# Kernel tuning notes

Measured on AMD Instinct MI355X. Metric: run time of the kernel, lower is better.

The kernel has to match this reference:

```python
import jax, jax.numpy as jnp
import numpy as np


def setup_inputs() -> dict:
    key = jax.random.key(0)
    ks = jax.random.split(key, 6)
    B, C, H, W = 4, 512, 64, 64
    Ci = C // 2
    x = jax.random.normal(ks[0], (B, C, H, W), dtype=jnp.float32)
    # 1x1 conv weights (kaiming-ish scale)
    wq = jax.random.normal(ks[1], (Ci, C), dtype=jnp.float32) * np.float32(np.sqrt(2.0 / C))
    wk = jax.random.normal(ks[2], (Ci, C), dtype=jnp.float32) * np.float32(np.sqrt(2.0 / C))
    wv = jax.random.normal(ks[3], (C, C), dtype=jnp.float32) * np.float32(np.sqrt(2.0 / C))
    bq = jnp.zeros((Ci,), jnp.float32)
    bk = jnp.zeros((Ci,), jnp.float32)
    bv = jnp.zeros((C,), jnp.float32)
    gamma_pam = jax.random.uniform(ks[4], (1,), dtype=jnp.float32)
    gamma_cam = jax.random.uniform(ks[5], (1,), dtype=jnp.float32)
    return {"x": x, "wq": wq, "bq": bq, "wk": wk, "bk": bk,
            "wv": wv, "bv": bv, "gamma_pam": gamma_pam, "gamma_cam": gamma_cam}


def reference(x, wq, bq, wk, bk, wv, bv, gamma_pam, gamma_cam):
    B, C, H, W = x.shape
    N = H * W
    xf = x.reshape(B, C, N)  # [B,C,N]

    # ---- PAM (position attention) ----
    q = jnp.einsum('oc,bcn->bon', wq, xf) + bq[None, :, None]  # [B,C/2,N]
    k = jnp.einsum('oc,bcn->bon', wk, xf) + bk[None, :, None]  # [B,C/2,N]
    v = jnp.einsum('oc,bcn->bon', wv, xf) + bv[None, :, None]  # [B,C,N]
    # energy[b,i,j] = sum_c q[b,c,i] k[b,c,j] / sqrt(C)
    energy = jnp.einsum('bci,bcj->bij', q, k) / jnp.sqrt(jnp.float32(C))
    attn = jax.nn.softmax(energy, axis=-1) / jnp.float32(N)  # [B,N,N]
    # out[b,c,i] = sum_j v[b,c,j] * attn[i,j]
    pam_out = jnp.einsum('bcj,bij->bci', v, attn)
    sa = jnp.tanh(gamma_pam[0] * pam_out + xf)  # [B,C,N]

    # ---- CAM (channel attention) on sa ----
    energy_c = jnp.einsum('bcn,bdn->bcd', sa, sa) / jnp.sqrt(jnp.float32(N))  # [B,C,C]
    energy_new = jnp.max(energy_c, axis=-1, keepdims=True) - energy_c
    attn_c = jax.nn.softmax(energy_new, axis=-1) / jnp.float32(C)
    cam_out = jnp.einsum('bcd,bdn->bcn', attn_c, sa)
    out = gamma_cam[0] * cam_out + sa
    return out.reshape(B, C, H, W)
```

## Files before the change

### kernel.cpp

```cpp
#include <hip/hip_runtime.h>

#define B_ 4
#define C_ 512
#define CI_ 256
#define N_ 4096
#define SCALE_PAM 0.04419417382415922f
#define SCALE_CAM (1.0f/64.0f)
#define SHIFT_PAM 8.0f

typedef float v4f __attribute__((ext_vector_type(4)));
typedef short v8s __attribute__((ext_vector_type(8)));

__device__ __forceinline__ unsigned short f2bf(float f) {
  unsigned int u = __float_as_uint(f);
  u = (u + 0x7FFFu + ((u >> 16) & 1u)) >> 16;
  return (unsigned short)u;
}
__device__ __forceinline__ float bf2f(unsigned short s) {
  return __uint_as_float(((unsigned int)s) << 16);
}
__device__ __forceinline__ v8s ld8(const unsigned short* p) {
  v8s r; *(int4*)&r = *(const int4*)p; return r;
}
__device__ __forceinline__ v4f mfma16(v8s a, v8s b, v4f c) {
  return __builtin_amdgcn_mfma_f32_16x16x32_bf16(a, b, c, 0, 0, 0);
}

__global__ __launch_bounds__(256) void k_wb(const float* __restrict__ wq,
                                            const float* __restrict__ wk,
                                            const float* __restrict__ wv,
                                            unsigned short* __restrict__ w_pk) {
  int u = blockIdx.x * 256 + threadIdx.x;
  int blk = u >> 6, wi = (u & 63) * 8;
  int r = (blk >> 4) * 16 + (wi >> 5);
  int k = (blk & 15) * 32 + (wi & 31);
  const float* src = (r < 256) ? &wq[r * 512 + k]
                   : (r < 512) ? &wk[(r - 256) * 512 + k]
                               : &wv[(r - 512) * 512 + k];
  float4 f0 = *(const float4*)src, f1 = *(const float4*)(src + 4);
  ushort4 o0 = { f2bf(f0.x), f2bf(f0.y), f2bf(f0.z), f2bf(f0.w) };
  ushort4 o1 = { f2bf(f1.x), f2bf(f1.y), f2bf(f1.z), f2bf(f1.w) };
  *(ushort4*)&w_pk[u * 8] = o0;
  *(ushort4*)&w_pk[u * 8 + 4] = o1;
}

__global__ __launch_bounds__(256) void k_xT(const float* __restrict__ x,
                                            unsigned short* __restrict__ x_pk) {
  const int b = blockIdx.z, c0 = blockIdx.y * 64, n0 = blockIdx.x * 64;
  const int t = threadIdx.x;
  __shared__ unsigned short ts[64 * 72];
  const int cl = t >> 2, nseg = (t & 3) * 16;
  const float* xr = x + ((size_t)b * C_ + c0 + cl) * N_ + n0 + nseg;
#pragma unroll
  for (int k = 0; k < 4; ++k) {
    float4 f = *(const float4*)(xr + k * 4);
    ts[(nseg + k * 4 + 0) * 72 + cl] = f2bf(f.x);
    ts[(nseg + k * 4 + 1) * 72 + cl] = f2bf(f.y);
    ts[(nseg + k * 4 + 2) * 72 + cl] = f2bf(f.z);
    ts[(nseg + k * 4 + 3) * 72 + cl] = f2bf(f.w);
  }
  __syncthreads();
  unsigned short* dst = x_pk + (size_t)b * N_ * C_;
#pragma unroll
  for (int u = t; u < 512; u += 256) {
    int blk = u >> 6, wi = (u & 63) * 8;
    int rl = (blk >> 1) * 16 + (wi >> 5);
    int kl = (blk & 1) * 32 + (wi & 31);
    int gr = n0 + rl, gk = c0 + kl;
    size_t go = ((size_t)(gr >> 4) * 16 + (gk >> 5)) * 512 + (gr & 15) * 32 + (gk & 31);
    *(int4*)&dst[go] = *(int4*)&ts[rl * 72 + kl];
  }
}

__global__ __launch_bounds__(512) void k_qkv(
    const unsigned short* __restrict__ w_pk, const unsigned short* __restrict__ x_pk,
    const float* __restrict__ bq, const float* __restrict__ bk, const float* __restrict__ bv,
    unsigned short* __restrict__ q_pk, unsigned short* __restrict__ k_pk,
    unsigned short* __restrict__ v_pk) {
  const int b = blockIdx.z, o0 = blockIdx.y * 128, n0 = blockIdx.x * 128;
  const int t = threadIdx.x, wave = t >> 6, lane = t & 63;
  const int la = lane & 15, quad = lane >> 4;
  const int ow = wave & 1, nw = wave >> 1;
  const int lanelin = la * 32 + quad * 8;
  const unsigned short* xpb = x_pk + (size_t)b * N_ * C_;
  __shared__ unsigned short tp[128 * 136];

  v4f acc[4][2];
#pragma unroll
  for (int i = 0; i < 4; ++i)
#pragma unroll
    for (int j = 0; j < 2; ++j) acc[i][j] = (v4f){0.f, 0.f, 0.f, 0.f};

  const int ar16 = (o0 + ow * 64) >> 4;
  const int br16 = (n0 + nw * 32) >> 4;
#pragma unroll 4
  for (int s = 0; s < 16; ++s) {
    v8s b0 = ld8(&xpb[((size_t)(br16 + 0) * 16 + s) * 512 + lanelin]);
    v8s b1 = ld8(&xpb[((size_t)(br16 + 1) * 16 + s) * 512 + lanelin]);
#pragma unroll
    for (int oi = 0; oi < 4; ++oi) {
      v8s a = ld8(&w_pk[((size_t)(ar16 + oi) * 16 + s) * 512 + lanelin]);
      acc[oi][0] = mfma16(a, b0, acc[oi][0]);
      acc[oi][1] = mfma16(a, b1, acc[oi][1]);
    }
  }

  if (o0 >= 512) {
#pragma unroll
    for (int oi = 0; oi < 4; ++oi)
#pragma unroll
      for (int nj = 0; nj < 2; ++nj)
#pragma unroll
        for (int r = 0; r < 4; ++r) {
          int cl = ow * 64 + oi * 16 + quad * 4 + r;
          int nl = nw * 32 + nj * 16 + la;
          tp[cl * 136 + nl] = f2bf(acc[oi][nj][r] + bv[o0 - 512 + cl]);
        }
    __syncthreads();
    unsigned short* dst = v_pk + (size_t)b * C_ * N_;
#pragma unroll
    for (int u = t; u < 2048; u += 512) {
      int blk = u >> 6, wi = (u & 63) * 8;
      int rl = (blk >> 2) * 16 + (wi >> 5);
      int kl = (blk & 3) * 32 + (wi & 31);
      int gr = (o0 - 512) + rl, gk = n0 + kl;
      size_t go = ((size_t)(gr >> 4) * 128 + (gk >> 5)) * 512 + (gr & 15) * 32 + (gk & 31);
      *(int4*)&dst[go] = *(int4*)&tp[rl * 136 + kl];
    }
  } else {
    const float* bias = (o0 < 256) ? bq : bk;
#pragma unroll
    for (int oi = 0; oi < 4; ++oi)
#pragma unroll
      for (int nj = 0; nj < 2; ++nj)
#pragma unroll
        for (int r = 0; r < 4; ++r) {
          int ol = ow * 64 + oi * 16 + quad * 4 + r;
          int nl = nw * 32 + nj * 16 + la;
          tp[nl * 136 + ol] = f2bf(acc[oi][nj][r] + bias[(o0 & 255) + ol]);
        }
    __syncthreads();
    unsigned short* dst = ((o0 < 256) ? q_pk : k_pk) + (size_t)b * N_ * CI_;
#pragma unroll
    for (int u = t; u < 2048; u += 512) {
      int blk = u >> 6, wi = (u & 63) * 8;
      int rl = (blk >> 2) * 16 + (wi >> 5);
      int kl = (blk & 3) * 32 + (wi & 31);
      int gr = n0 + rl, gk = (o0 & 255) + kl;
      size_t go = ((size_t)(gr >> 4) * 8 + (gk >> 5)) * 512 + (gr & 15) * 32 + (gk & 31);
      *(int4*)&dst[go] = *(int4*)&tp[rl * 136 + kl];
    }
  }
}

__device__ __forceinline__ void kstage(const unsigned short* g, unsigned short* l, int t) {
  __builtin_amdgcn_global_load_lds(
      (const __attribute__((address_space(1))) void*)(g + (size_t)t * 8),
      (__attribute__((address_space(3))) void*)(l + t * 8), 16, 0, 0);
  __builtin_amdgcn_global_load_lds(
      (const __attribute__((address_space(1))) void*)(g + 8192 + (size_t)t * 8),
      (__attribute__((address_space(3))) void*)(l + 8192 + t * 8), 16, 0, 0);
}

__global__ __launch_bounds__(1024) void k_pam(
    const unsigned short* __restrict__ q_pk, const unsigned short* __restrict__ k_pk,
    const unsigned short* __restrict__ v_pk, const float* __restrict__ x,
    const float* __restrict__ gamma_pam,
    unsigned short* __restrict__ sa_pk, unsigned short* __restrict__ saT_pk) {
  const int blk = blockIdx.x;
  const int b = blk & 3, i0 = (blk >> 2) * 64;
  const int t = threadIdx.x, wave = t >> 6, lane = t & 63;
  const int la = lane & 15, quad = lane >> 4;
  const int iw = wave & 3, jw = wave >> 2;
  const int cb = wave * 32;
  const int lanelin = la * 32 + quad * 8;

  __shared__ unsigned short kls[3][16384];
  __shared__ unsigned short pa[2][4096];
  __shared__ float l_lds[64];
  if (t < 64) l_lds[t] = 0.f;

  const unsigned short* qpk = q_pk + (size_t)b * N_ * CI_;
  const unsigned short* kpk = k_pk + (size_t)b * N_ * CI_;
  const unsigned short* vpk = v_pk + (size_t)b * C_ * N_;

  v8s qf[8];
  {
    const unsigned short* qb = qpk + ((size_t)((i0 >> 4) + iw) * 8) * 512 + lanelin;
#pragma unroll
    for (int s = 0; s < 8; ++s) qf[s] = ld8(qb + s * 512);
  }

  v4f acc[2][4];
#pragma unroll
  for (int ct = 0; ct < 2; ++ct)
#pragma unroll
    for (int it = 0; it < 4; ++it) acc[ct][it] = (v4f){0.f, 0.f, 0.f, 0.f};
  float lsum[4] = {0.f, 0.f, 0.f, 0.f};

  kstage(kpk, kls[0], t);
  kstage(kpk + (size_t)4 * 4096, kls[1], t);
  asm volatile("s_waitcnt vmcnt(2)" ::: "memory");
  __builtin_amdgcn_s_barrier();
  __builtin_amdgcn_sched_barrier(0);

  int pb = 0;
  for (int step = 0; step < 64; ++step) {
    const int j0 = step * 64;
    v8s vf[2][2];
#pragma unroll
    for (int ct = 0; ct < 2; ++ct)
#pragma unroll
      for (int ks = 0; ks < 2; ++ks)
        vf[ct][ks] = ld8(&vpk[((size_t)((cb >> 4) + ct) * 128 + (j0 >> 5) + ks) * 512 + lanelin]);
    __builtin_amdgcn_sched_barrier(0);
    int jn = j0 + 128; if (jn >= N_) jn = 0;
    kstage(kpk + (size_t)(jn >> 4) * 4096, kls[(step + 2) % 3], t);
    __builtin_amdgcn_sched_barrier(0);
    const unsigned short* kb = &kls[step % 3][jw * 4096 + lanelin];
    v4f sA = (v4f){0.f, 0.f, 0.f, 0.f}, sB = sA;
#pragma unroll
    for (int sh = 0; sh < 4; ++sh) {
      sA = mfma16(qf[sh], ld8(kb + sh * 512), sA);
      sB = mfma16(qf[sh + 4], ld8(kb + (sh + 4) * 512), sB);
    }
#pragma unroll
    for (int r = 0; r < 4; ++r) {
      float p = __expf((sA[r] + sB[r]) * SCALE_PAM - SHIFT_PAM);
      lsum[r] += p;
      int row = iw * 16 + quad * 4 + r;
      pa[pb][((row << 6) + jw * 16 + la) ^ ((row & 7) << 3)] = f2bf(p);
    }
    __builtin_amdgcn_sched_barrier(0);
    asm volatile("s_waitcnt lgkmcnt(0) vmcnt(6)" ::: "memory");
    __builtin_amdgcn_s_barrier();
    __builtin_amdgcn_sched_barrier(0);
    __builtin_amdgcn_s_setprio(1);
#pragma unroll
    for (int it = 0; it < 4; ++it) {
      const int row = it * 16 + la;
      const int sw = (row & 7) << 3;
#pragma unroll
      for (int ks = 0; ks < 2; ++ks) {
        v8s pf; *(int4*)&pf = *(const int4*)&pa[pb][((row << 6) + ks * 32 + quad * 8) ^ sw];
#pragma unroll
        for (int ct = 0; ct < 2; ++ct)
          acc[ct][it] = mfma16(vf[ct][ks], pf, acc[ct][it]);
      }
    }
    __builtin_amdgcn_s_setprio(0);
    pb ^= 1;
  }

#pragma unroll
  for (int r = 0; r < 4; ++r) {
    float v = lsum[r];
    v += __shfl_xor(v, 1); v += __shfl_xor(v, 2);
    v += __shfl_xor(v, 4); v += __shfl_xor(v, 8);
    if (la == 0) atomicAdd(&l_lds[iw * 16 + quad * 4 + r], v);
  }
  __syncthreads();

  const float gpv = gamma_pam[0];
  unsigned short* ts = &kls[0][0];
  unsigned short sv[2][4][4];
#pragma unroll
  for (int ct = 0; ct < 2; ++ct)
#pragma unroll
    for (int it = 0; it < 4; ++it) {
      const int nl = it * 16 + la;
      const float lv = l_lds[nl] * (float)N_;
#pragma unroll
      for (int r = 0; r < 4; ++r) {
        const int c = cb + ct * 16 + quad * 4 + r;
        const float xv = x[((size_t)b * C_ + c) * N_ + i0 + nl];
        const unsigned short h = f2bf(tanhf(fmaf(gpv, acc[ct][it][r] / lv, xv)));
        sv[ct][it][r] = h;
        ts[c * 72 + nl] = h;
      }
    }
  __syncthreads();
  {
    unsigned short* dst = sa_pk + (size_t)b * C_ * N_;
#pragma unroll
    for (int u = t; u < 4096; u += 1024) {
      int c = u >> 3, n8 = (u & 7) * 8;
      int gn = i0 + n8;
      size_t go = ((size_t)(c >> 4) * 128 + (gn >> 5)) * 512 + (c & 15) * 32 + (gn & 31);
      *(int4*)&dst[go] = *(const int4*)&ts[c * 72 + n8];
    }
  }
  __syncthreads();
  unsigned short* ts2 = &kls[0][0];
#pragma unroll
  for (int ct = 0; ct < 2; ++ct)
#pragma unroll
    for (int it = 0; it < 4; ++it)
#pragma unroll
      for (int r = 0; r < 4; ++r)
        ts2[(it * 16 + la) * 520 + (cb + ct * 16 + quad * 4 + r)] = sv[ct][it][r];
  __syncthreads();
  {
    unsigned short* dst = saT_pk + (size_t)b * N_ * C_;
#pragma unroll
    for (int u = t; u < 4096; u += 1024) {
      int nl = u >> 6, c8 = (u & 63) * 8;
      int gn = i0 + nl;
      size_t go = ((size_t)(gn >> 4) * 16 + (c8 >> 5)) * 512 + (gn & 15) * 32 + (c8 & 31);
      *(int4*)&dst[go] = *(const int4*)&ts2[nl * 520 + c8];
    }
  }
}

__global__ __launch_bounds__(256) void k_cam_e(const unsigned short* __restrict__ sa_pk,
                                               float* __restrict__ e_part) {
  const int b = blockIdx.z, ks = blockIdx.y;
  const int c0 = (blockIdx.x & 7) * 64, d0 = (blockIdx.x >> 3) * 64;
  const int t = threadIdx.x, wave = t >> 6, lane = t & 63;
  const int la = lane & 15, quad = lane >> 4;
  const int cw = wave & 1, dw = wave >> 1;
  const int lanelin = la * 32 + quad * 8;
  const unsigned short* sb = sa_pk + (size_t)b * C_ * N_;

  v4f acc[2][2];
#pragma unroll
  for (int i = 0; i < 2; ++i)
#pragma unroll
    for (int j = 0; j < 2; ++j) acc[i][j] = (v4f){0.f, 0.f, 0.f, 0.f};

  const int ar16 = (c0 + cw * 32) >> 4;
  const int br16 = (d0 + dw * 32) >> 4;
#pragma unroll 4
  for (int s = 0; s < 32; ++s) {
    const int k32 = ks * 32 + s;
    v8s a0 = ld8(&sb[((size_t)(ar16 + 0) * 128 + k32) * 512 + lanelin]);
    v8s a1 = ld8(&sb[((size_t)(ar16 + 1) * 128 + k32) * 512 + lanelin]);
    v8s b0 = ld8(&sb[((size_t)(br16 + 0) * 128 + k32) * 512 + lanelin]);
    v8s b1 = ld8(&sb[((size_t)(br16 + 1) * 128 + k32) * 512 + lanelin]);
    acc[0][0] = mfma16(a0, b0, acc[0][0]);
    acc[0][1] = mfma16(a0, b1, acc[0][1]);
    acc[1][0] = mfma16(a1, b0, acc[1][0]);
    acc[1][1] = mfma16(a1, b1, acc[1][1]);
  }
  float* ep = e_part + ((size_t)(ks * B_ + b)) * C_ * C_;
#pragma unroll
  for (int i = 0; i < 2; ++i)
#pragma unroll
    for (int j = 0; j < 2; ++j)
#pragma unroll
      for (int r = 0; r < 4; ++r) {
        int c = c0 + cw * 32 + i * 16 + quad * 4 + r;
        int d = d0 + dw * 32 + j * 16 + la;
        ep[(size_t)c * C_ + d] = acc[i][j][r] * SCALE_CAM;
      }
}

__global__ __launch_bounds__(64) void k_cam_softmax(const float* __restrict__ e_part,
                                                    unsigned short* __restrict__ attn_pk) {
  const int c = blockIdx.x, b = blockIdx.y, lane = threadIdx.x;
  size_t roff = ((size_t)b * C_ + c) * C_;
  float vals[8];
#pragma unroll
  for (int r = 0; r < 8; ++r) {
    int d = lane + r * 64;
    float s = 0.f;
#pragma unroll
    for (int p = 0; p < 4; ++p) s += e_part[(size_t)(p * B_) * C_ * C_ + roff + d];
    vals[r] = s;
  }
  float mn = vals[0];
#pragma unroll
  for (int r = 1; r < 8; ++r) mn = fminf(mn, vals[r]);
#pragma unroll
  for (int m = 32; m >= 1; m >>= 1) mn = fminf(mn, __shfl_xor(mn, m));
  float sum = 0.f;
#pragma unroll
  for (int r = 0; r < 8; ++r) { vals[r] = __expf(mn - vals[r]); sum += vals[r]; }
#pragma unroll
  for (int m = 32; m >= 1; m >>= 1) sum += __shfl_xor(sum, m);
  float sc = (1.0f / (float)C_) / sum;
  unsigned short* ab = attn_pk + (size_t)b * C_ * C_;
#pragma unroll
  for (int r = 0; r < 8; ++r) {
    int d = lane + r * 64;
    size_t go = ((size_t)(c >> 4) * 16 + (d >> 5)) * 512 + (c & 15) * 32 + (d & 31);
    ab[go] = f2bf(vals[r] * sc);
  }
}

__global__ __launch_bounds__(512) void k_cam_out(
    const unsigned short* __restrict__ attn_pk, const unsigned short* __restrict__ saT_pk,
    const unsigned short* __restrict__ sa_pk, const float* __restrict__ gamma_cam,
    float* __restrict__ out) {
  const int b = blockIdx.z, c0 = blockIdx.y * 128, n0 = blockIdx.x * 128;
  const int t = threadIdx.x, wave = t >> 6, lane = t & 63;
  const int la = lane & 15, quad = lane >> 4;
  const int cw = wave & 1, nw = wave >> 1;
  const int lanelin = la * 32 + quad * 8;
  const unsigned short* ab = attn_pk + (size_t)b * C_ * C_;
  const unsigned short* sTb = saT_pk + (size_t)b * N_ * C_;
  const unsigned short* sb = sa_pk + (size_t)b * C_ * N_;

  v4f acc[4][2];
#pragma unroll
  for (int i = 0; i < 4; ++i)
#pragma unroll
    for (int j = 0; j < 2; ++j) acc[i][j] = (v4f){0.f, 0.f, 0.f, 0.f};

  const int ar16 = (c0 + cw * 64) >> 4;
  const int br16 = (n0 + nw * 32) >> 4;
#pragma unroll 4
  for (int s = 0; s < 16; ++s) {
    v8s b0 = ld8(&sTb[((size_t)(br16 + 0) * 16 + s) * 512 + lanelin]);
    v8s b1 = ld8(&sTb[((size_t)(br16 + 1) * 16 + s) * 512 + lanelin]);
#pragma unroll
    for (int ci = 0; ci < 4; ++ci) {
      v8s a = ld8(&ab[((size_t)(ar16 + ci) * 16 + s) * 512 + lanelin]);
      acc[ci][0] = mfma16(a, b0, acc[ci][0]);
      acc[ci][1] = mfma16(a, b1, acc[ci][1]);
    }
  }
  const float gc = gamma_cam[0];
#pragma unroll
  for (int ci = 0; ci < 4; ++ci)
#pragma unroll
    for (int nj = 0; nj < 2; ++nj)
#pragma unroll
      for (int r = 0; r < 4; ++r) {
        int c = c0 + cw * 64 + ci * 16 + quad * 4 + r;
        int n = n0 + nw * 32 + nj * 16 + la;
        size_t pko = ((size_t)(c >> 4) * 128 + (n >> 5)) * 512 + (c & 15) * 32 + (n & 31);
        out[((size_t)b * C_ + c) * N_ + n] = fmaf(gc, acc[ci][nj][r], bf2f(sb[pko]));
      }
}

extern "C" void kernel_launch(void* const* d_in, const int* in_sizes, int n_in,
                              void* d_out, int out_size, void* d_ws, size_t ws_size,
                              hipStream_t stream) {
  const float* x  = (const float*)d_in[0];
  const float* wq = (const float*)d_in[1];
  const float* bq = (const float*)d_in[2];
  const float* wk = (const float*)d_in[3];
  const float* bk = (const float*)d_in[4];
  const float* wv = (const float*)d_in[5];
  const float* bv = (const float*)d_in[6];
  const float* gp = (const float*)d_in[7];
  const float* gc = (const float*)d_in[8];
  float* out = (float*)d_out;

  char* ws = (char*)d_ws;
  unsigned short* x_pk   = (unsigned short*)(ws);
  unsigned short* w_pk   = (unsigned short*)(ws + 16777216);
  unsigned short* q_pk   = (unsigned short*)(ws + 17825792);
  unsigned short* k_pk   = (unsigned short*)(ws + 26214400);
  unsigned short* v_pk   = (unsigned short*)(ws + 34603008);
  unsigned short* sa_pk  = (unsigned short*)(ws + 51380224);
  unsigned short* saT_pk = (unsigned short*)(ws + 68157440);
  float*          ep     = (float*)(ws + 34603008);
  unsigned short* at_pk  = (unsigned short*)(ws);

  k_xT<<<dim3(64, 8, B_), 256, 0, stream>>>(x, x_pk);
  k_wb<<<256, 256, 0, stream>>>(wq, wk, wv, w_pk);
  k_qkv<<<dim3(32, 8, B_), 512, 0, stream>>>(w_pk, x_pk, bq, bk, bv, q_pk, k_pk, v_pk);
  k_pam<<<256, 1024, 0, stream>>>(q_pk, k_pk, v_pk, x, gp, sa_pk, saT_pk);
  k_cam_e<<<dim3(64, 4, B_), 256, 0, stream>>>(sa_pk, ep);
  k_cam_softmax<<<dim3(C_, B_), 64, 0, stream>>>(ep, at_pk);
  k_cam_out<<<dim3(32, 4, B_), 512, 0, stream>>>(at_pk, saT_pk, sa_pk, gc, out);
}
```

Before: 360.9 us.

## Fuse CAM softmax into energy kernel using shift-free exp and deferred normalization

Removes the split-K partial energy buffer and the separate CAM softmax kernel. The energy kernel now does full-K accumulation, writes exp(-e) directly as bf16 attention, and atomically accumulates per-row sums. The output kernel divides by the row sum and folds in gamma and 1/C. This drops the max-subtraction by relying on the bounded range of tanh outputs, and it reduces grid parallelism in the energy kernel.

```diff
diff --git a/kernel.cpp b/kernel.cpp
--- a/kernel.cpp
+++ b/kernel.cpp
@@ -29,7 +29,9 @@
 __global__ __launch_bounds__(256) void k_wb(const float* __restrict__ wq,
                                             const float* __restrict__ wk,
                                             const float* __restrict__ wv,
-                                            unsigned short* __restrict__ w_pk) {
+                                            unsigned short* __restrict__ w_pk,
+                                            float* __restrict__ rsum) {
+  if (blockIdx.x < 8) rsum[blockIdx.x * 256 + threadIdx.x] = 0.f;
   int u = blockIdx.x * 256 + threadIdx.x;
   int blk = u >> 6, wi = (u & 63) * 8;
   int r = (blk >> 4) * 16 + (wi >> 5);
@@ -313,8 +315,9 @@
 }
 
 __global__ __launch_bounds__(256) void k_cam_e(const unsigned short* __restrict__ sa_pk,
-                                               float* __restrict__ e_part) {
-  const int b = blockIdx.z, ks = blockIdx.y;
+                                               unsigned short* __restrict__ attn_pk,
+                                               float* __restrict__ rsum) {
+  const int b = blockIdx.y;
   const int c0 = (blockIdx.x & 7) * 64, d0 = (blockIdx.x >> 3) * 64;
   const int t = threadIdx.x, wave = t >> 6, lane = t & 63;
   const int la = lane & 15, quad = lane >> 4;
@@ -331,67 +334,42 @@
   const int ar16 = (c0 + cw * 32) >> 4;
   const int br16 = (d0 + dw * 32) >> 4;
 #pragma unroll 4
-  for (int s = 0; s < 32; ++s) {
-    const int k32 = ks * 32 + s;
-    v8s a0 = ld8(&sb[((size_t)(ar16 + 0) * 128 + k32) * 512 + lanelin]);
-    v8s a1 = ld8(&sb[((size_t)(ar16 + 1) * 128 + k32) * 512 + lanelin]);
-    v8s b0 = ld8(&sb[((size_t)(br16 + 0) * 128 + k32) * 512 + lanelin]);
-    v8s b1 = ld8(&sb[((size_t)(br16 + 1) * 128 + k32) * 512 + lanelin]);
+  for (int s = 0; s < 128; ++s) {
+    v8s a0 = ld8(&sb[((size_t)(ar16 + 0) * 128 + s) * 512 + lanelin]);
+    v8s a1 = ld8(&sb[((size_t)(ar16 + 1) * 128 + s) * 512 + lanelin]);
+    v8s b0 = ld8(&sb[((size_t)(br16 + 0) * 128 + s) * 512 + lanelin]);
+    v8s b1 = ld8(&sb[((size_t)(br16 + 1) * 128 + s) * 512 + lanelin]);
     acc[0][0] = mfma16(a0, b0, acc[0][0]);
     acc[0][1] = mfma16(a0, b1, acc[0][1]);
     acc[1][0] = mfma16(a1, b0, acc[1][0]);
     acc[1][1] = mfma16(a1, b1, acc[1][1]);
   }
-  float* ep = e_part + ((size_t)(ks * B_ + b)) * C_ * C_;
+  unsigned short* ab = attn_pk + (size_t)b * C_ * C_;
+  float* rs = rsum + b * C_;
 #pragma unroll
   for (int i = 0; i < 2; ++i)
 #pragma unroll
-    for (int j = 0; j < 2; ++j)
-#pragma unroll
-      for (int r = 0; r < 4; ++r) {
-        int c = c0 + cw * 32 + i * 16 + quad * 4 + r;
+    for (int r = 0; r < 4; ++r) {
+      const int c = c0 + cw * 32 + i * 16 + quad * 4 + r;
+      float psum = 0.f;
+#pragma unroll
+      for (int j = 0; j < 2; ++j) {
+        float p = __expf(-acc[i][j][r] * SCALE_CAM);
+        psum += p;
         int d = d0 + dw * 32 + j * 16 + la;
-        ep[(size_t)c * C_ + d] = acc[i][j][r] * SCALE_CAM;
+        size_t go = ((size_t)(c >> 4) * 16 + (d >> 5)) * 512 + (c & 15) * 32 + (d & 31);
+        ab[go] = f2bf(p);
       }
-}
-
-__global__ __launch_bounds__(64) void k_cam_softmax(const float* __restrict__ e_part,
-                                                    unsigned short* __restrict__ attn_pk) {
-  const int c = blockIdx.x, b = blockIdx.y, lane = threadIdx.x;
-  size_t roff = ((size_t)b * C_ + c) * C_;
-  float vals[8];
-#pragma unroll
-  for (int r = 0; r < 8; ++r) {
-    int d = lane + r * 64;
-    float s = 0.f;
-#pragma unroll
-    for (int p = 0; p < 4; ++p) s += e_part[(size_t)(p * B_) * C_ * C_ + roff + d];
-    vals[r] = s;
-  }
-  float mn = vals[0];
-#pragma unroll
-  for (int r = 1; r < 8; ++r) mn = fminf(mn, vals[r]);
-#pragma unroll
-  for (int m = 32; m >= 1; m >>= 1) mn = fminf(mn, __shfl_xor(mn, m));
-  float sum = 0.f;
-#pragma unroll
-  for (int r = 0; r < 8; ++r) { vals[r] = __expf(mn - vals[r]); sum += vals[r]; }
-#pragma unroll
-  for (int m = 32; m >= 1; m >>= 1) sum += __shfl_xor(sum, m);
-  float sc = (1.0f / (float)C_) / sum;
-  unsigned short* ab = attn_pk + (size_t)b * C_ * C_;
-#pragma unroll
-  for (int r = 0; r < 8; ++r) {
-    int d = lane + r * 64;
-    size_t go = ((size_t)(c >> 4) * 16 + (d >> 5)) * 512 + (c & 15) * 32 + (d & 31);
-    ab[go] = f2bf(vals[r] * sc);
-  }
+      psum += __shfl_xor(psum, 1); psum += __shfl_xor(psum, 2);
+      psum += __shfl_xor(psum, 4); psum += __shfl_xor(psum, 8);
+      if (la == 0) atomicAdd(&rs[c], psum);
+    }
 }
 
 __global__ __launch_bounds__(512) void k_cam_out(
     const unsigned short* __restrict__ attn_pk, const unsigned short* __restrict__ saT_pk,
     const unsigned short* __restrict__ sa_pk, const float* __restrict__ gamma_cam,
-    float* __restrict__ out) {
+    const float* __restrict__ rsum, float* __restrict__ out) {
   const int b = blockIdx.z, c0 = blockIdx.y * 128, n0 = blockIdx.x * 128;
   const int t = threadIdx.x, wave = t >> 6, lane = t & 63;
   const int la = lane & 15, quad = lane >> 4;
@@ -420,7 +398,8 @@
       acc[ci][1] = mfma16(a, b1, acc[ci][1]);
     }
   }
-  const float gc = gamma_cam[0];
+  const float gcs = gamma_cam[0] * (1.0f / (float)C_);
+  const float* rs = rsum + b * C_;
 #pragma unroll
   for (int ci = 0; ci < 4; ++ci)
 #pragma unroll
@@ -429,8 +408,9 @@
       for (int r = 0; r < 4; ++r) {
         int c = c0 + cw * 64 + ci * 16 + quad * 4 + r;
         int n = n0 + nw * 32 + nj * 16 + la;
+        float sc = gcs / rs[c];
         size_t pko = ((size_t)(c >> 4) * 128 + (n >> 5)) * 512 + (c & 15) * 32 + (n & 31);
-        out[((size_t)b * C_ + c) * N_ + n] = fmaf(gc, acc[ci][nj][r], bf2f(sb[pko]));
+        out[((size_t)b * C_ + c) * N_ + n] = fmaf(sc, acc[ci][nj][r], bf2f(sb[pko]));
       }
 }
 
@@ -456,14 +436,13 @@
   unsigned short* v_pk   = (unsigned short*)(ws + 34603008);
   unsigned short* sa_pk  = (unsigned short*)(ws + 51380224);
   unsigned short* saT_pk = (unsigned short*)(ws + 68157440);
-  float*          ep     = (float*)(ws + 34603008);
+  float*          rsum   = (float*)(ws + 84934656);
   unsigned short* at_pk  = (unsigned short*)(ws);
 
   k_xT<<<dim3(64, 8, B_), 256, 0, stream>>>(x, x_pk);
-  k_wb<<<256, 256, 0, stream>>>(wq, wk, wv, w_pk);
+  k_wb<<<256, 256, 0, stream>>>(wq, wk, wv, w_pk, rsum);
   k_qkv<<<dim3(32, 8, B_), 512, 0, stream>>>(w_pk, x_pk, bq, bk, bv, q_pk, k_pk, v_pk);
   k_pam<<<256, 1024, 0, stream>>>(q_pk, k_pk, v_pk, x, gp, sa_pk, saT_pk);
-  k_cam_e<<<dim3(64, 4, B_), 256, 0, stream>>>(sa_pk, ep);
-  k_cam_softmax<<<dim3(C_, B_), 64, 0, stream>>>(ep, at_pk);
-  k_cam_out<<<dim3(32, 4, B_), 512, 0, stream>>>(at_pk, saT_pk, sa_pk, gc, out);
-}
+  k_cam_e<<<dim3(64, B_), 256, 0, stream>>>(sa_pk, at_pk, rsum);
+  k_cam_out<<<dim3(32, 4, B_), 512, 0, stream>>>(at_pk, saT_pk, sa_pk, gc, rsum, out);
+}
```

Result: slower. 368.6 us (+2.1%).
